# Optimization experiments

Measured on AMD Instinct MI355X. Metric: run time of the kernel, lower is better.

The kernel has to match this reference:

```python
import jax, jax.numpy as jnp
import numpy as np

N = 100_000   # entities
E = 1_000_000 # edges (triples)
R = 1_000     # relations
D = 100       # node_hidden
DEPTH = 2
EPS = 1e-12


def _segment_mean(vals, idx, num):
    s = jax.ops.segment_sum(vals, idx, num_segments=num)
    cnt = jax.ops.segment_sum(jnp.ones((vals.shape[0],), vals.dtype), idx, num_segments=num)
    return s / jnp.maximum(cnt, 1.0)[:, None]


def _edge_softmax(logits, dst, num):
    # softmax over edges grouped by destination node
    m = jax.ops.segment_max(logits, dst, num_segments=num)
    e = jnp.exp(logits - m[dst])
    s = jax.ops.segment_sum(e, dst, num_segments=num)
    return e / s[dst]


def _rrea_encoder(features, rel_emb, src, dst, erel, kernels):
    feats = jnp.tanh(features)
    outs = [feats]
    for l in range(DEPTH):
        rels = rel_emb[erel]                                        # [E, D]
        rels = rels / jnp.maximum(jnp.linalg.norm(rels, axis=1, keepdims=True), EPS)
        neighs = feats[src]                                         # [E, D]
        selfs = feats[dst]                                          # [E, D]
        # Householder reflection of neighbor features about relation direction
        neighs = neighs - 2.0 * jnp.sum(neighs * rels, axis=1, keepdims=True) * rels
        k = kernels[l]                                              # [3D, 1]
        w_s, w_n, w_r = k[:D, 0], k[D:2 * D, 0], k[2 * D:, 0]
        logits = selfs @ w_s + neighs @ w_n + rels @ w_r            # [E]
        att = _edge_softmax(logits, dst, N)
        feats = jax.ops.segment_sum(neighs * att[:, None], dst, num_segments=N)
        feats = jnp.tanh(feats)
        outs.append(feats)
    return jnp.concatenate(outs, axis=1)                            # [N, (DEPTH+1)*D]


def setup_inputs() -> dict:
    key = jax.random.key(0)
    k1, k2, k3, k4, k5, k6, k7 = jax.random.split(key, 7)
    ent_emb = jax.random.uniform(k1, (N, D), jnp.float32, -0.05, 0.05)
    rel_emb = jax.random.uniform(k2, (R, D), jnp.float32, -0.05, 0.05)
    attn_e = jax.random.normal(k3, (DEPTH, 3 * D, 1), jnp.float32)
    attn_r = jax.random.normal(k4, (DEPTH, 3 * D, 1), jnp.float32)
    src = jax.random.randint(k5, (E,), 0, N, jnp.int32)
    dst = jnp.sort(jax.random.randint(k6, (E,), 0, N, jnp.int32))
    erel = jax.random.randint(k7, (E,), 0, R, jnp.int32)
    return {"ent_emb": ent_emb, "rel_emb": rel_emb, "attn_e": attn_e,
            "attn_r": attn_r, "src": src, "dst": dst, "erel": erel}


def reference(ent_emb, rel_emb, attn_e, attn_r, src, dst, erel):
    # initial entity feature: mean of in-neighbor entity embeddings
    ent_feature = _segment_mean(ent_emb[src], dst, N)               # [N, D]
    # initial relation feature per entity: mean of incident relation embeddings
    rel_feature = _segment_mean(rel_emb[erel], dst, N)              # [N, D]
    out_ent = _rrea_encoder(ent_feature, rel_emb, src, dst, erel, attn_e)
    out_rel = _rrea_encoder(rel_feature, rel_emb, src, dst, erel, attn_r)
    # dropout_rate=0.0 / eval mode -> identity
    return jnp.concatenate([out_ent, out_rel], axis=-1)             # [N, 2*(DEPTH+1)*D]
```

## Files before the change

kernel.cpp:

```cpp
#include <hip/hip_runtime.h>
#include <hip/hip_fp16.h>
#include <math.h>

#define NN 100000
#define NE 1000000
#define NR 1000
#define DD 100
#define HS 104
#define FS2 208
#define OUTC 600
#define EPS 1e-12f
#define NBIN 64
#define RESCALE_THR 8.0f

struct __attribute__((aligned(16))) h8 { unsigned short u[8]; };

__device__ inline float h2f(unsigned short u) {
    __half_raw r; r.x = u; __half h = r; return __half2float(h);
}
__device__ inline unsigned short f2h(float f) {
    __half h = __float2half_rn(f); __half_raw r = h; return r.x;
}

__device__ inline float wave_sum(float v) {
#pragma unroll
    for (int o = 32; o > 0; o >>= 1) v += __shfl_down(v, o, 64);
    return __shfl(v, 0, 64);
}
__device__ inline float quad_sum(float v) {
    v += __shfl_xor(v, 1, 64);
    v += __shfl_xor(v, 2, 64);
    return v;
}

__global__ void k_rowptr(const int* __restrict__ dst, int* __restrict__ row_ptr,
                         int* __restrict__ ghist) {
    int n = blockIdx.x * blockDim.x + threadIdx.x;
    if (n < NBIN) ghist[n] = 0;
    if (n > NN) return;
    int lo = 0, hi = NE;
    while (lo < hi) {
        int mid = (lo + hi) >> 1;
        if (dst[mid] < n) lo = mid + 1; else hi = mid;
    }
    row_ptr[n] = lo;
}

__global__ void k_hist(const int* __restrict__ row_ptr, int* __restrict__ ghist) {
    __shared__ int lh[NBIN];
    int t = threadIdx.x;
    if (t < NBIN) lh[t] = 0;
    __syncthreads();
    int n = blockIdx.x * blockDim.x + t;
    if (n < NN) {
        int d = row_ptr[n + 1] - row_ptr[n];
        atomicAdd(&lh[min(d, NBIN - 1)], 1);
    }
    __syncthreads();
    if (t < NBIN && lh[t]) atomicAdd(&ghist[t], lh[t]);
}
__global__ void k_scan(const int* __restrict__ ghist, int* __restrict__ goffs) {
    if (threadIdx.x == 0) {
        int s = 0;
        for (int i = 0; i < NBIN; ++i) { goffs[i] = s; s += ghist[i]; }
    }
}
__global__ void k_scatter(const int* __restrict__ row_ptr, int* __restrict__ goffs,
                          int* __restrict__ perm) {
    __shared__ int lh[NBIN], base[NBIN];
    int t = threadIdx.x;
    if (t < NBIN) lh[t] = 0;
    __syncthreads();
    int n = blockIdx.x * blockDim.x + t;
    int bin = 0, rank = 0;
    if (n < NN) {
        int d = row_ptr[n + 1] - row_ptr[n];
        bin = min(d, NBIN - 1);
        rank = atomicAdd(&lh[bin], 1);
    }
    __syncthreads();
    if (t < NBIN && lh[t]) base[t] = atomicAdd(&goffs[t], lh[t]);
    __syncthreads();
    if (n < NN) perm[base[bin] + rank] = n;
}

__global__ void k_relnorm(const float* __restrict__ rel_emb, float* __restrict__ rel_norm,
                          unsigned short* __restrict__ rel_nh) {
    int w = (blockIdx.x * blockDim.x + threadIdx.x) >> 6;
    int lane = threadIdx.x & 63;
    if (w >= NR) return;
    const float* r = rel_emb + w * DD;
    float v0 = r[lane];
    float v1 = (lane + 64 < DD) ? r[lane + 64] : 0.f;
    float ss = wave_sum(v0 * v0 + v1 * v1);
    float sc = 1.f / fmaxf(sqrtf(ss), EPS);
    float* o = rel_norm + w * DD;
    unsigned short* oh = rel_nh + (size_t)w * HS;
    o[lane] = v0 * sc;
    oh[lane] = f2h(v0 * sc);
    if (lane + 64 < DD) {
        o[lane + 64] = v1 * sc;
        oh[lane + 64] = f2h(v1 * sc);
    }
}

__global__ void k_relv2(const float* __restrict__ rel_norm,
                        const float* __restrict__ k3dA, const float* __restrict__ k3dB,
                        float4* __restrict__ rrP) {
    int w = (blockIdx.x * blockDim.x + threadIdx.x) >> 6;
    int lane = threadIdx.x & 63;
    if (w >= NR) return;
    const float* r = rel_norm + w * DD;
    float r0 = r[lane];
    float r1 = (lane + 64 < DD) ? r[lane + 64] : 0.f;
    float wrA0 = k3dA[2 * DD + lane], wnA0 = k3dA[DD + lane];
    float wrB0 = k3dB[2 * DD + lane], wnB0 = k3dB[DD + lane];
    float wrA1 = 0.f, wnA1 = 0.f, wrB1 = 0.f, wnB1 = 0.f;
    if (lane + 64 < DD) {
        wrA1 = k3dA[2 * DD + lane + 64]; wnA1 = k3dA[DD + lane + 64];
        wrB1 = k3dB[2 * DD + lane + 64]; wnB1 = k3dB[DD + lane + 64];
    }
    float rdA = wave_sum(r0 * wrA0 + r1 * wrA1);
    float rdB = wave_sum(r0 * wrB0 + r1 * wrB1);
    float rnA = wave_sum(r0 * wnA0 + r1 * wnA1);
    float rnB = wave_sum(r0 * wnB0 + r1 * wnB1);
    if (lane == 0) { float4 v = { rdA, rdB, rnA, rnB }; rrP[w] = v; }
}


__global__ __launch_bounds__(256) void k_segmean2(
        const float* __restrict__ ent_emb, const float* __restrict__ rel_emb,
        const int* __restrict__ src, const int* __restrict__ erel,
        const int* __restrict__ row_ptr, const int* __restrict__ perm,
        const float* __restrict__ k3dA, const float* __restrict__ k3dB,
        float2* __restrict__ sdP, float2* __restrict__ ndP,
        unsigned short* __restrict__ fused_out,
        float* __restrict__ out) {
    int gi = (blockIdx.x * blockDim.x + threadIdx.x) >> 2;
    int sb = threadIdx.x & 3;
    if (gi >= NN) return;
    int n = perm[gi];
    int beg = row_ptr[n], end = row_ptr[n + 1];
    float a0[25] = {}, a1[25] = {};
    for (int e = beg; e < end; ++e) {
        int s = src[e];
        int t = erel[e];
        const float* er = ent_emb + (size_t)s * DD;
        const float* rr = rel_emb + (size_t)t * DD;
        const float4* e4 = (const float4*)er;
        const float4* r4 = (const float4*)rr;
#pragma unroll
        for (int k = 0; k < 6; ++k) {
            float4 v = e4[6 * sb + k];
            a0[4 * k] += v.x; a0[4 * k + 1] += v.y; a0[4 * k + 2] += v.z; a0[4 * k + 3] += v.w;
            float4 u = r4[6 * sb + k];
            a1[4 * k] += u.x; a1[4 * k + 1] += u.y; a1[4 * k + 2] += u.z; a1[4 * k + 3] += u.w;
        }
        a0[24] += er[96 + sb];
        a1[24] += rr[96 + sb];
    }
    float inv = 1.f / fmaxf((float)(end - beg), 1.f);
    float o0[25], o1[25];
#pragma unroll
    for (int m = 0; m < 25; ++m) { o0[m] = tanhf(a0[m] * inv); o1[m] = tanhf(a1[m] * inv); }
    if (fused_out) {
        unsigned short* fr = fused_out + (size_t)n * FS2;
#pragma unroll
        for (int j = 0; j < 3; ++j) {
            h8 x, y;
#pragma unroll
            for (int m = 0; m < 8; ++m) { x.u[m] = f2h(o0[8 * j + m]); y.u[m] = f2h(o1[8 * j + m]); }
            ((h8*)(fr + 24 * sb))[j] = x;
            ((h8*)(fr + 104 + 24 * sb))[j] = y;
        }
        fr[96 + sb] = f2h(o0[24]);
        fr[200 + sb] = f2h(o1[24]);
    }
    float* oc = out + (size_t)n * OUTC;
    float4* oc4 = (float4*)oc;
    float4* od4 = (float4*)(oc + 300);
#pragma unroll
    for (int k = 0; k < 6; ++k) {
        float4 v = { o0[4 * k], o0[4 * k + 1], o0[4 * k + 2], o0[4 * k + 3] };
        oc4[6 * sb + k] = v;
        float4 u = { o1[4 * k], o1[4 * k + 1], o1[4 * k + 2], o1[4 * k + 3] };
        od4[6 * sb + k] = u;
    }
    oc[96 + sb] = o0[24];
    oc[300 + 96 + sb] = o1[24];
    float sp0 = o0[24] * k3dA[96 + sb], np0 = o0[24] * k3dA[DD + 96 + sb];
    float sp1 = o1[24] * k3dB[96 + sb], np1 = o1[24] * k3dB[DD + 96 + sb];
    const float4* wA = (const float4*)k3dA;
    const float4* wAn = (const float4*)(k3dA + DD);
    const float4* wB = (const float4*)k3dB;
    const float4* wBn = (const float4*)(k3dB + DD);
#pragma unroll
    for (int k = 0; k < 6; ++k) {
        float4 ws = wA[6 * sb + k], wn = wAn[6 * sb + k];
        sp0 += o0[4 * k] * ws.x + o0[4 * k + 1] * ws.y + o0[4 * k + 2] * ws.z + o0[4 * k + 3] * ws.w;
        np0 += o0[4 * k] * wn.x + o0[4 * k + 1] * wn.y + o0[4 * k + 2] * wn.z + o0[4 * k + 3] * wn.w;
        float4 vs = wB[6 * sb + k], vn = wBn[6 * sb + k];
        sp1 += o1[4 * k] * vs.x + o1[4 * k + 1] * vs.y + o1[4 * k + 2] * vs.z + o1[4 * k + 3] * vs.w;
        np1 += o1[4 * k] * vn.x + o1[4 * k + 1] * vn.y + o1[4 * k + 2] * vn.z + o1[4 * k + 3] * vn.w;
    }
    sp0 = quad_sum(sp0); np0 = quad_sum(np0);
    sp1 = quad_sum(sp1); np1 = quad_sum(np1);
    if (sb == 0) {
        float2 sv = { sp0, sp1 }; sdP[n] = sv;
        float2 nv = { np0, np1 }; ndP[n] = nv;
    }
}

template<int SRC>
__global__ __launch_bounds__(256) void k_layer2(
        const void* __restrict__ Fin,
        const unsigned short* __restrict__ rel_nh,
        const int* __restrict__ src, const int* __restrict__ erel,
        const int* __restrict__ row_ptr, const int* __restrict__ perm,
        const float2* __restrict__ sdP, const float2* __restrict__ ndP,
        const float4* __restrict__ rrP,
        const float* __restrict__ k3dA_next, const float* __restrict__ k3dB_next,
        float2* __restrict__ sdP_o, float2* __restrict__ ndP_o,
        unsigned short* __restrict__ fused_out,
        float* __restrict__ out, int ocol) {
    int gi = (blockIdx.x * blockDim.x + threadIdx.x) >> 2;
    int sb = threadIdx.x & 3;
    if (gi >= NN) return;
    int n = perm[gi];
    int beg = row_ptr[n], end = row_ptr[n + 1];
    float2 sd2 = sdP[n];
    float acc0[25] = {}, acc1[25] = {};
    float m0 = -INFINITY, l0 = 0.f, m1 = -INFINITY, l1 = 0.f;
    for (int e = beg; e < end; ++e) {
        int s = src[e];
        int r = erel[e];
        float2 nd2 = ndP[s];
        float4 rr = rrP[r];
        float f0[25], f1[25], rv[25];
        if (SRC == 0) {
            const unsigned short* fr = (const unsigned short*)Fin + (size_t)s * FS2;
            const h8* p = (const h8*)(fr + 24 * sb);
            const h8* q = (const h8*)(fr + 104 + 24 * sb);
            h8 x0 = p[0], x1 = p[1], x2 = p[2];
            h8 y0 = q[0], y1 = q[1], y2 = q[2];
#pragma unroll
            for (int m = 0; m < 8; ++m) {
                f0[m] = h2f(x0.u[m]); f0[8 + m] = h2f(x1.u[m]); f0[16 + m] = h2f(x2.u[m]);
                f1[m] = h2f(y0.u[m]); f1[8 + m] = h2f(y1.u[m]); f1[16 + m] = h2f(y2.u[m]);
            }
            f0[24] = h2f(fr[96 + sb]);
            f1[24] = h2f(fr[200 + sb]);
        } else {
            const float* fr = (const float*)Fin + (size_t)s * OUTC;
            const float4* a4 = (const float4*)fr;
            const float4* b4 = (const float4*)(fr + 300);
#pragma unroll
            for (int k = 0; k < 6; ++k) {
                float4 v = a4[6 * sb + k];
                f0[4 * k] = v.x; f0[4 * k + 1] = v.y; f0[4 * k + 2] = v.z; f0[4 * k + 3] = v.w;
                float4 u = b4[6 * sb + k];
                f1[4 * k] = u.x; f1[4 * k + 1] = u.y; f1[4 * k + 2] = u.z; f1[4 * k + 3] = u.w;
            }
            f0[24] = fr[96 + sb];
            f1[24] = fr[300 + 96 + sb];
        }
        const unsigned short* rh = rel_nh + (size_t)r * HS;
        const h8* rp = (const h8*)(rh + 24 * sb);
        h8 z0 = rp[0], z1 = rp[1], z2 = rp[2];
#pragma unroll
        for (int m = 0; m < 8; ++m) {
            rv[m] = h2f(z0.u[m]); rv[8 + m] = h2f(z1.u[m]); rv[16 + m] = h2f(z2.u[m]);
        }
        rv[24] = h2f(rh[96 + sb]);
        float p0 = f0[24] * rv[24], p1 = f1[24] * rv[24];
#pragma unroll
        for (int m = 0; m < 24; ++m) { p0 += f0[m] * rv[m]; p1 += f1[m] * rv[m]; }
        p0 = quad_sum(p0);
        p1 = quad_sum(p1);
        float c0 = 2.f * p0, c1 = 2.f * p1;
        float lg0 = sd2.x + nd2.x - c0 * rr.z + rr.x;
        float lg1 = sd2.y + nd2.y - c1 * rr.w + rr.y;
        float w0, w1;
        if (lg0 > m0 + RESCALE_THR) {
            float sc = __expf(m0 - lg0);
            l0 *= sc;
#pragma unroll
            for (int m = 0; m < 25; ++m) acc0[m] *= sc;
            m0 = lg0; w0 = 1.f;
        } else w0 = __expf(lg0 - m0);
        if (lg1 > m1 + RESCALE_THR) {
            float sc = __expf(m1 - lg1);
            l1 *= sc;
#pragma unroll
            for (int m = 0; m < 25; ++m) acc1[m] *= sc;
            m1 = lg1; w1 = 1.f;
        } else w1 = __expf(lg1 - m1);
        l0 += w0; l1 += w1;
        float wc0 = w0 * c0, wc1 = w1 * c1;
#pragma unroll
        for (int m = 0; m < 25; ++m) {
            acc0[m] += w0 * f0[m] - wc0 * rv[m];
            acc1[m] += w1 * f1[m] - wc1 * rv[m];
        }
    }
    float i0 = (end > beg) ? (1.f / l0) : 0.f;
    float i1 = (end > beg) ? (1.f / l1) : 0.f;
    float o0[25], o1[25];
#pragma unroll
    for (int m = 0; m < 25; ++m) { o0[m] = tanhf(acc0[m] * i0); o1[m] = tanhf(acc1[m] * i1); }
    if (fused_out) {
        unsigned short* fr = fused_out + (size_t)n * FS2;
#pragma unroll
        for (int j = 0; j < 3; ++j) {
            h8 x, y;
#pragma unroll
            for (int m = 0; m < 8; ++m) { x.u[m] = f2h(o0[8 * j + m]); y.u[m] = f2h(o1[8 * j + m]); }
            ((h8*)(fr + 24 * sb))[j] = x;
            ((h8*)(fr + 104 + 24 * sb))[j] = y;
        }
        fr[96 + sb] = f2h(o0[24]);
        fr[200 + sb] = f2h(o1[24]);
    }
    float* oc = out + (size_t)n * OUTC + ocol;
    float4* oc4 = (float4*)oc;
    float4* od4 = (float4*)(oc + 300);
#pragma unroll
    for (int k = 0; k < 6; ++k) {
        float4 v = { o0[4 * k], o0[4 * k + 1], o0[4 * k + 2], o0[4 * k + 3] };
        oc4[6 * sb + k] = v;
        float4 u = { o1[4 * k], o1[4 * k + 1], o1[4 * k + 2], o1[4 * k + 3] };
        od4[6 * sb + k] = u;
    }
    oc[96 + sb] = o0[24];
    oc[300 + 96 + sb] = o1[24];
    if (k3dA_next) {
        float sp0 = o0[24] * k3dA_next[96 + sb], np0 = o0[24] * k3dA_next[DD + 96 + sb];
        float sp1 = o1[24] * k3dB_next[96 + sb], np1 = o1[24] * k3dB_next[DD + 96 + sb];
        const float4* wA = (const float4*)k3dA_next;
        const float4* wAn = (const float4*)(k3dA_next + DD);
        const float4* wB = (const float4*)k3dB_next;
        const float4* wBn = (const float4*)(k3dB_next + DD);
#pragma unroll
        for (int k = 0; k < 6; ++k) {
            float4 ws = wA[6 * sb + k], wn = wAn[6 * sb + k];
            sp0 += o0[4 * k] * ws.x + o0[4 * k + 1] * ws.y + o0[4 * k + 2] * ws.z + o0[4 * k + 3] * ws.w;
            np0 += o0[4 * k] * wn.x + o0[4 * k + 1] * wn.y + o0[4 * k + 2] * wn.z + o0[4 * k + 3] * wn.w;
            float4 vs = wB[6 * sb + k], vn = wBn[6 * sb + k];
            sp1 += o1[4 * k] * vs.x + o1[4 * k + 1] * vs.y + o1[4 * k + 2] * vs.z + o1[4 * k + 3] * vs.w;
            np1 += o1[4 * k] * vn.x + o1[4 * k + 1] * vn.y + o1[4 * k + 2] * vn.z + o1[4 * k + 3] * vn.w;
        }
        sp0 = quad_sum(sp0); np0 = quad_sum(np0);
        sp1 = quad_sum(sp1); np1 = quad_sum(np1);
        if (sb == 0) {
            float2 sv = { sp0, sp1 }; sdP_o[n] = sv;
            float2 nv = { np0, np1 }; ndP_o[n] = nv;
        }
    }
}

extern "C" void kernel_launch(void* const* d_in, const int* in_sizes, int n_in,
                              void* d_out, int out_size, void* d_ws, size_t ws_size,
                              hipStream_t stream) {
    const float* ent_emb = (const float*)d_in[0];
    const float* rel_emb = (const float*)d_in[1];
    const float* attn_e  = (const float*)d_in[2];
    const float* attn_r  = (const float*)d_in[3];
    const int*   src     = (const int*)d_in[4];
    const int*   dst     = (const int*)d_in[5];
    const int*   erel    = (const int*)d_in[6];
    float* out = (float*)d_out;

    char* ws = (char*)d_ws;
    size_t off = 0;
    auto alloc = [&](size_t bytes) -> void* {
        void* p = ws + off;
        off = (off + bytes + 255) & ~(size_t)255;
        return p;
    };
    int*    row_ptr  = (int*)alloc((NN + 1) * sizeof(int));
    float*  rel_norm = (float*)alloc((size_t)NR * DD * sizeof(float));
    unsigned short* rel_nh = (unsigned short*)alloc((size_t)NR * HS * sizeof(unsigned short));
    float2* sdPA = (float2*)alloc(NN * sizeof(float2));
    float2* ndPA = (float2*)alloc(NN * sizeof(float2));
    float2* sdPB = (float2*)alloc(NN * sizeof(float2));
    float2* ndPB = (float2*)alloc(NN * sizeof(float2));
    float4* rrP0 = (float4*)alloc(NR * sizeof(float4));
    float4* rrP1 = (float4*)alloc(NR * sizeof(float4));
    int*    ghist = (int*)alloc(NBIN * sizeof(int));
    int*    goffs = (int*)alloc(NBIN * sizeof(int));
    int*    perm  = (int*)alloc(NN * sizeof(int));
    unsigned short* fusedA = (unsigned short*)alloc((size_t)NN * FS2 * sizeof(unsigned short));
    bool planB = (off <= ws_size);
    unsigned short* fusedB = (unsigned short*)alloc((size_t)NN * FS2 * sizeof(unsigned short));
    bool planA = (off <= ws_size);

    hipLaunchKernelGGL(k_rowptr, dim3((NN + 256) / 256), dim3(256), 0, stream,
                       dst, row_ptr, ghist);
    hipLaunchKernelGGL(k_hist, dim3((NN + 255) / 256), dim3(256), 0, stream, row_ptr, ghist);
    hipLaunchKernelGGL(k_scan, dim3(1), dim3(64), 0, stream, ghist, goffs);
    hipLaunchKernelGGL(k_scatter, dim3((NN + 255) / 256), dim3(256), 0, stream,
                       row_ptr, goffs, perm);
    hipLaunchKernelGGL(k_relnorm, dim3(NR * 64 / 256), dim3(256), 0, stream,
                       rel_emb, rel_norm, rel_nh);
    hipLaunchKernelGGL(k_relv2, dim3(NR * 64 / 256), dim3(256), 0, stream,
                       rel_norm, attn_e, attn_r, rrP0);
    hipLaunchKernelGGL(k_relv2, dim3(NR * 64 / 256), dim3(256), 0, stream,
                       rel_norm, attn_e + 300, attn_r + 300, rrP1);

    const int NODE_BLOCKS = (NN + 63) / 64;

    hipLaunchKernelGGL(k_segmean2, dim3(NODE_BLOCKS), dim3(256), 0, stream,
                       ent_emb, rel_emb, src, erel, row_ptr, perm,
                       attn_e, attn_r, sdPA, ndPA,
                       planB ? fusedA : (unsigned short*)nullptr, out);

    if (planB) {
        hipLaunchKernelGGL(HIP_KERNEL_NAME(k_layer2<0>), dim3(NODE_BLOCKS), dim3(256), 0, stream,
                           (const void*)fusedA, rel_nh, src, erel, row_ptr, perm,
                           sdPA, ndPA, rrP0, attn_e + 300, attn_r + 300,
                           sdPB, ndPB,
                           planA ? fusedB : (unsigned short*)nullptr, out, 100);
    } else {
        hipLaunchKernelGGL(HIP_KERNEL_NAME(k_layer2<1>), dim3(NODE_BLOCKS), dim3(256), 0, stream,
                           (const void*)out, rel_nh, src, erel, row_ptr, perm,
                           sdPA, ndPA, rrP0, attn_e + 300, attn_r + 300,
                           sdPB, ndPB,
                           (unsigned short*)nullptr, out, 100);
    }

    if (planA) {
        hipLaunchKernelGGL(HIP_KERNEL_NAME(k_layer2<0>), dim3(NODE_BLOCKS), dim3(256), 0, stream,
                           (const void*)fusedB, rel_nh, src, erel, row_ptr, perm,
                           sdPB, ndPB, rrP1, (const float*)nullptr, (const float*)nullptr,
                           sdPB, ndPB,
                           (unsigned short*)nullptr, out, 200);
    } else {
        hipLaunchKernelGGL(HIP_KERNEL_NAME(k_layer2<1>), dim3(NODE_BLOCKS), dim3(256), 0, stream,
                           (const void*)(out + 100), rel_nh, src, erel, row_ptr, perm,
                           sdPB, ndPB, rrP1, (const float*)nullptr, (const float*)nullptr,
                           sdPB, ndPB,
                           (unsigned short*)nullptr, out, 200);
    }
}
```

Baseline: 760.6 us.

## Pack edge indices, gather fp16 embeddings, and schedule nodes via atomic work queue

```diff
diff --git a/kernel.cpp b/kernel.cpp
--- a/kernel.cpp
+++ b/kernel.cpp
@@ -12,6 +12,7 @@
 #define EPS 1e-12f
 #define NBIN 64
 #define RESCALE_THR 8.0f
+#define NWCH (NN / 16)
 
 struct __attribute__((aligned(16))) h8 { unsigned short u[8]; };
 
@@ -59,10 +60,12 @@
     __syncthreads();
     if (t < NBIN && lh[t]) atomicAdd(&ghist[t], lh[t]);
 }
-__global__ void k_scan(const int* __restrict__ ghist, int* __restrict__ goffs) {
+__global__ void k_scan(const int* __restrict__ ghist, int* __restrict__ goffs,
+                       int* __restrict__ ctrs) {
     if (threadIdx.x == 0) {
         int s = 0;
         for (int i = 0; i < NBIN; ++i) { goffs[i] = s; s += ghist[i]; }
+        ctrs[0] = 0; ctrs[1] = 0; ctrs[2] = 0;
     }
 }
 __global__ void k_scatter(const int* __restrict__ row_ptr, int* __restrict__ goffs,
@@ -82,6 +85,13 @@
     if (t < NBIN && lh[t]) base[t] = atomicAdd(&goffs[t], lh[t]);
     __syncthreads();
     if (n < NN) perm[base[bin] + rank] = n;
+}
+
+__global__ void k_pack(const int* __restrict__ src, const int* __restrict__ erel,
+                       unsigned int* __restrict__ ep) {
+    int e = blockIdx.x * blockDim.x + threadIdx.x;
+    if (e >= NE) return;
+    ep[e] = (unsigned int)src[e] | ((unsigned int)erel[e] << 17);
 }
 
 __global__ void k_relnorm(const float* __restrict__ rel_emb, float* __restrict__ rel_norm,
@@ -127,219 +137,101 @@
     if (lane == 0) { float4 v = { rdA, rdB, rnA, rnB }; rrP[w] = v; }
 }
 
+__global__ void k_tohalf(const float* __restrict__ s, unsigned short* __restrict__ d, int rows) {
+    int gi = blockIdx.x * blockDim.x + threadIdx.x;
+    int n = gi >> 2, sb = gi & 3;
+    if (n >= rows) return;
+    const float4* s4 = (const float4*)(s + (size_t)n * DD);
+    unsigned short* dr = d + (size_t)n * HS;
+#pragma unroll
+    for (int j = 0; j < 3; ++j) {
+        float4 a = s4[6 * sb + 2 * j];
+        float4 b = s4[6 * sb + 2 * j + 1];
+        h8 o;
+        o.u[0] = f2h(a.x); o.u[1] = f2h(a.y); o.u[2] = f2h(a.z); o.u[3] = f2h(a.w);
+        o.u[4] = f2h(b.x); o.u[5] = f2h(b.y); o.u[6] = f2h(b.z); o.u[7] = f2h(b.w);
+        ((h8*)(dr + 24 * sb))[j] = o;
+    }
+    dr[96 + sb] = f2h(s[(size_t)n * DD + 96 + sb]);
+}
+
 
 __global__ __launch_bounds__(256) void k_segmean2(
-        const float* __restrict__ ent_emb, const float* __restrict__ rel_emb,
-        const int* __restrict__ src, const int* __restrict__ erel,
+        const unsigned short* __restrict__ ent_h, const unsigned short* __restrict__ rel_eh,
+        const unsigned int* __restrict__ ep,
         const int* __restrict__ row_ptr, const int* __restrict__ perm,
         const float* __restrict__ k3dA, const float* __restrict__ k3dB,
         float2* __restrict__ sdP, float2* __restrict__ ndP,
         unsigned short* __restrict__ fused_out,
-        float* __restrict__ out) {
-    int gi = (blockIdx.x * blockDim.x + threadIdx.x) >> 2;
-    int sb = threadIdx.x & 3;
-    if (gi >= NN) return;
-    int n = perm[gi];
-    int beg = row_ptr[n], end = row_ptr[n + 1];
-    float a0[25] = {}, a1[25] = {};
-    for (int e = beg; e < end; ++e) {
-        int s = src[e];
-        int t = erel[e];
-        const float* er = ent_emb + (size_t)s * DD;
-        const float* rr = rel_emb + (size_t)t * DD;
-        const float4* e4 = (const float4*)er;
-        const float4* r4 = (const float4*)rr;
+        float* __restrict__ out, int* __restrict__ ctr) {
+    int lane = threadIdx.x & 63;
+    int qi = lane >> 2, sb = lane & 3;
+    for (;;) {
+        int t;
+        if (lane == 0) t = atomicAdd(ctr, 1);
+        t = __shfl(t, 0, 64);
+        if (t >= NWCH) break;
+        int gi = (NWCH - 1 - t) * 16 + qi;
+        int n = perm[gi];
+        int beg = row_ptr[n], end = row_ptr[n + 1];
+        float a0[25] = {}, a1[25] = {};
+        for (int e = beg; e < end; ++e) {
+            unsigned int v = ep[e];
+            int s = v & 0x1FFFF;
+            int r = v >> 17;
+            const unsigned short* er = ent_h + (size_t)s * HS;
+            const unsigned short* rr = rel_eh + (size_t)r * HS;
+            const h8* e8 = (const h8*)(er + 24 * sb);
+            const h8* r8 = (const h8*)(rr + 24 * sb);
+            h8 xa = e8[0], xb = e8[1], xc = e8[2];
+            h8 ya = r8[0], yb = r8[1], yc = r8[2];
+#pragma unroll
+            for (int m = 0; m < 8; ++m) {
+                a0[m]      += h2f(xa.u[m]);
+                a0[8 + m]  += h2f(xb.u[m]);
+                a0[16 + m] += h2f(xc.u[m]);
+                a1[m]      += h2f(ya.u[m]);
+                a1[8 + m]  += h2f(yb.u[m]);
+                a1[16 + m] += h2f(yc.u[m]);
+            }
+            a0[24] += h2f(er[96 + sb]);
+            a1[24] += h2f(rr[96 + sb]);
+        }
+        float inv = 1.f / fmaxf((float)(end - beg), 1.f);
+        float o0[25], o1[25];
+#pragma unroll
+        for (int m = 0; m < 25; ++m) { o0[m] = tanhf(a0[m] * inv); o1[m] = tanhf(a1[m] * inv); }
+        if (fused_out) {
+            unsigned short* fr = fused_out + (size_t)n * FS2;
+#pragma unroll
+            for (int j = 0; j < 3; ++j) {
+                h8 x, y;
+#pragma unroll
+                for (int m = 0; m < 8; ++m) { x.u[m] = f2h(o0[8 * j + m]); y.u[m] = f2h(o1[8 * j + m]); }
+                ((h8*)(fr + 24 * sb))[j] = x;
+                ((h8*)(fr + 104 + 24 * sb))[j] = y;
+            }
+            fr[96 + sb] = f2h(o0[24]);
+            fr[200 + sb] = f2h(o1[24]);
+        }
+        float* oc = out + (size_t)n * OUTC;
+        float4* oc4 = (float4*)oc;
+        float4* od4 = (float4*)(oc + 300);
 #pragma unroll
         for (int k = 0; k < 6; ++k) {
-            float4 v = e4[6 * sb + k];
-            a0[4 * k] += v.x; a0[4 * k + 1] += v.y; a0[4 * k + 2] += v.z; a0[4 * k + 3] += v.w;
-            float4 u = r4[6 * sb + k];
-            a1[4 * k] += u.x; a1[4 * k + 1] += u.y; a1[4 * k + 2] += u.z; a1[4 * k + 3] += u.w;
-        }
-        a0[24] += er[96 + sb];
-        a1[24] += rr[96 + sb];
-    }
-    float inv = 1.f / fmaxf((float)(end - beg), 1.f);
-    float o0[25], o1[25];
-#pragma unroll
-    for (int m = 0; m < 25; ++m) { o0[m] = tanhf(a0[m] * inv); o1[m] = tanhf(a1[m] * inv); }
-    if (fused_out) {
-        unsigned short* fr = fused_out + (size_t)n * FS2;
-#pragma unroll
-        for (int j = 0; j < 3; ++j) {
-            h8 x, y;
-#pragma unroll
-            for (int m = 0; m < 8; ++m) { x.u[m] = f2h(o0[8 * j + m]); y.u[m] = f2h(o1[8 * j + m]); }
-            ((h8*)(fr + 24 * sb))[j] = x;
-            ((h8*)(fr + 104 + 24 * sb))[j] = y;
-        }
-        fr[96 + sb] = f2h(o0[24]);
-        fr[200 + sb] = f2h(o1[24]);
-    }
-    float* oc = out + (size_t)n * OUTC;
-    float4* oc4 = (float4*)oc;
-    float4* od4 = (float4*)(oc + 300);
-#pragma unroll
-    for (int k = 0; k < 6; ++k) {
-        float4 v = { o0[4 * k], o0[4 * k + 1], o0[4 * k + 2], o0[4 * k + 3] };
-        oc4[6 * sb + k] = v;
-        float4 u = { o1[4 * k], o1[4 * k + 1], o1[4 * k + 2], o1[4 * k + 3] };
-        od4[6 * sb + k] = u;
-    }
-    oc[96 + sb] = o0[24];
-    oc[300 + 96 + sb] = o1[24];
-    float sp0 = o0[24] * k3dA[96 + sb], np0 = o0[24] * k3dA[DD + 96 + sb];
-    float sp1 = o1[24] * k3dB[96 + sb], np1 = o1[24] * k3dB[DD + 96 + sb];
-    const float4* wA = (const float4*)k3dA;
-    const float4* wAn = (const float4*)(k3dA + DD);
-    const float4* wB = (const float4*)k3dB;
-    const float4* wBn = (const float4*)(k3dB + DD);
-#pragma unroll
-    for (int k = 0; k < 6; ++k) {
-        float4 ws = wA[6 * sb + k], wn = wAn[6 * sb + k];
-        sp0 += o0[4 * k] * ws.x + o0[4 * k + 1] * ws.y + o0[4 * k + 2] * ws.z + o0[4 * k + 3] * ws.w;
-        np0 += o0[4 * k] * wn.x + o0[4 * k + 1] * wn.y + o0[4 * k + 2] * wn.z + o0[4 * k + 3] * wn.w;
-        float4 vs = wB[6 * sb + k], vn = wBn[6 * sb + k];
-        sp1 += o1[4 * k] * vs.x + o1[4 * k + 1] * vs.y + o1[4 * k + 2] * vs.z + o1[4 * k + 3] * vs.w;
-        np1 += o1[4 * k] * vn.x + o1[4 * k + 1] * vn.y + o1[4 * k + 2] * vn.z + o1[4 * k + 3] * vn.w;
-    }
-    sp0 = quad_sum(sp0); np0 = quad_sum(np0);
-    sp1 = quad_sum(sp1); np1 = quad_sum(np1);
-    if (sb == 0) {
-        float2 sv = { sp0, sp1 }; sdP[n] = sv;
-        float2 nv = { np0, np1 }; ndP[n] = nv;
-    }
-}
-
-template<int SRC>
-__global__ __launch_bounds__(256) void k_layer2(
-        const void* __restrict__ Fin,
-        const unsigned short* __restrict__ rel_nh,
-        const int* __restrict__ src, const int* __restrict__ erel,
-        const int* __restrict__ row_ptr, const int* __restrict__ perm,
-        const float2* __restrict__ sdP, const float2* __restrict__ ndP,
-        const float4* __restrict__ rrP,
-        const float* __restrict__ k3dA_next, const float* __restrict__ k3dB_next,
-        float2* __restrict__ sdP_o, float2* __restrict__ ndP_o,
-        unsigned short* __restrict__ fused_out,
-        float* __restrict__ out, int ocol) {
-    int gi = (blockIdx.x * blockDim.x + threadIdx.x) >> 2;
-    int sb = threadIdx.x & 3;
-    if (gi >= NN) return;
-    int n = perm[gi];
-    int beg = row_ptr[n], end = row_ptr[n + 1];
-    float2 sd2 = sdP[n];
-    float acc0[25] = {}, acc1[25] = {};
-    float m0 = -INFINITY, l0 = 0.f, m1 = -INFINITY, l1 = 0.f;
-    for (int e = beg; e < end; ++e) {
-        int s = src[e];
-        int r = erel[e];
-        float2 nd2 = ndP[s];
-        float4 rr = rrP[r];
-        float f0[25], f1[25], rv[25];
-        if (SRC == 0) {
-            const unsigned short* fr = (const unsigned short*)Fin + (size_t)s * FS2;
-            const h8* p = (const h8*)(fr + 24 * sb);
-            const h8* q = (const h8*)(fr + 104 + 24 * sb);
-            h8 x0 = p[0], x1 = p[1], x2 = p[2];
-            h8 y0 = q[0], y1 = q[1], y2 = q[2];
-#pragma unroll
-            for (int m = 0; m < 8; ++m) {
-                f0[m] = h2f(x0.u[m]); f0[8 + m] = h2f(x1.u[m]); f0[16 + m] = h2f(x2.u[m]);
-                f1[m] = h2f(y0.u[m]); f1[8 + m] = h2f(y1.u[m]); f1[16 + m] = h2f(y2.u[m]);
-            }
-            f0[24] = h2f(fr[96 + sb]);
-            f1[24] = h2f(fr[200 + sb]);
-        } else {
-            const float* fr = (const float*)Fin + (size_t)s * OUTC;
-            const float4* a4 = (const float4*)fr;
-            const float4* b4 = (const float4*)(fr + 300);
-#pragma unroll
-            for (int k = 0; k < 6; ++k) {
-                float4 v = a4[6 * sb + k];
-                f0[4 * k] = v.x; f0[4 * k + 1] = v.y; f0[4 * k + 2] = v.z; f0[4 * k + 3] = v.w;
-                float4 u = b4[6 * sb + k];
-                f1[4 * k] = u.x; f1[4 * k + 1] = u.y; f1[4 * k + 2] = u.z; f1[4 * k + 3] = u.w;
-            }
-            f0[24] = fr[96 + sb];
-            f1[24] = fr[300 + 96 + sb];
-        }
-        const unsigned short* rh = rel_nh + (size_t)r * HS;
-        const h8* rp = (const h8*)(rh + 24 * sb);
-        h8 z0 = rp[0], z1 = rp[1], z2 = rp[2];
-#pragma unroll
-        for (int m = 0; m < 8; ++m) {
-            rv[m] = h2f(z0.u[m]); rv[8 + m] = h2f(z1.u[m]); rv[16 + m] = h2f(z2.u[m]);
-        }
-        rv[24] = h2f(rh[96 + sb]);
-        float p0 = f0[24] * rv[24], p1 = f1[24] * rv[24];
-#pragma unroll
-        for (int m = 0; m < 24; ++m) { p0 += f0[m] * rv[m]; p1 += f1[m] * rv[m]; }
-        p0 = quad_sum(p0);
-        p1 = quad_sum(p1);
-        float c0 = 2.f * p0, c1 = 2.f * p1;
-        float lg0 = sd2.x + nd2.x - c0 * rr.z + rr.x;
-        float lg1 = sd2.y + nd2.y - c1 * rr.w + rr.y;
-        float w0, w1;
-        if (lg0 > m0 + RESCALE_THR) {
-            float sc = __expf(m0 - lg0);
-            l0 *= sc;
-#pragma unroll
-            for (int m = 0; m < 25; ++m) acc0[m] *= sc;
-            m0 = lg0; w0 = 1.f;
-        } else w0 = __expf(lg0 - m0);
-        if (lg1 > m1 + RESCALE_THR) {
-            float sc = __expf(m1 - lg1);
-            l1 *= sc;
-#pragma unroll
-            for (int m = 0; m < 25; ++m) acc1[m] *= sc;
-            m1 = lg1; w1 = 1.f;
-        } else w1 = __expf(lg1 - m1);
-        l0 += w0; l1 += w1;
-        float wc0 = w0 * c0, wc1 = w1 * c1;
-#pragma unroll
-        for (int m = 0; m < 25; ++m) {
-            acc0[m] += w0 * f0[m] - wc0 * rv[m];
-            acc1[m] += w1 * f1[m] - wc1 * rv[m];
-        }
-    }
-    float i0 = (end > beg) ? (1.f / l0) : 0.f;
-    float i1 = (end > beg) ? (1.f / l1) : 0.f;
-    float o0[25], o1[25];
-#pragma unroll
-    for (int m = 0; m < 25; ++m) { o0[m] = tanhf(acc0[m] * i0); o1[m] = tanhf(acc1[m] * i1); }
-    if (fused_out) {
-        unsigned short* fr = fused_out + (size_t)n * FS2;
-#pragma unroll
-        for (int j = 0; j < 3; ++j) {
-            h8 x, y;
-#pragma unroll
-            for (int m = 0; m < 8; ++m) { x.u[m] = f2h(o0[8 * j + m]); y.u[m] = f2h(o1[8 * j + m]); }
-            ((h8*)(fr + 24 * sb))[j] = x;
-            ((h8*)(fr + 104 + 24 * sb))[j] = y;
-        }
-        fr[96 + sb] = f2h(o0[24]);
-        fr[200 + sb] = f2h(o1[24]);
-    }
-    float* oc = out + (size_t)n * OUTC + ocol;
-    float4* oc4 = (float4*)oc;
-    float4* od4 = (float4*)(oc + 300);
-#pragma unroll
-    for (int k = 0; k < 6; ++k) {
-        float4 v = { o0[4 * k], o0[4 * k + 1], o0[4 * k + 2], o0[4 * k + 3] };
-        oc4[6 * sb + k] = v;
-        float4 u = { o1[4 * k], o1[4 * k + 1], o1[4 * k + 2], o1[4 * k + 3] };
-        od4[6 * sb + k] = u;
-    }
-    oc[96 + sb] = o0[24];
-    oc[300 + 96 + sb] = o1[24];
-    if (k3dA_next) {
-        float sp0 = o0[24] * k3dA_next[96 + sb], np0 = o0[24] * k3dA_next[DD + 96 + sb];
-        float sp1 = o1[24] * k3dB_next[96 + sb], np1 = o1[24] * k3dB_next[DD + 96 + sb];
-        const float4* wA = (const float4*)k3dA_next;
-        const float4* wAn = (const float4*)(k3dA_next + DD);
-        const float4* wB = (const float4*)k3dB_next;
-        const float4* wBn = (const float4*)(k3dB_next + DD);
+            float4 v0 = { o0[4 * k], o0[4 * k + 1], o0[4 * k + 2], o0[4 * k + 3] };
+            oc4[6 * sb + k] = v0;
+            float4 u0 = { o1[4 * k], o1[4 * k + 1], o1[4 * k + 2], o1[4 * k + 3] };
+            od4[6 * sb + k] = u0;
+        }
+        oc[96 + sb] = o0[24];
+        oc[300 + 96 + sb] = o1[24];
+        float sp0 = o0[24] * k3dA[96 + sb], np0 = o0[24] * k3dA[DD + 96 + sb];
+        float sp1 = o1[24] * k3dB[96 + sb], np1 = o1[24] * k3dB[DD + 96 + sb];
+        const float4* wA = (const float4*)k3dA;
+        const float4* wAn = (const float4*)(k3dA + DD);
+        const float4* wB = (const float4*)k3dB;
+        const float4* wBn = (const float4*)(k3dB + DD);
 #pragma unroll
         for (int k = 0; k < 6; ++k) {
             float4 ws = wA[6 * sb + k], wn = wAn[6 * sb + k];
@@ -352,8 +244,162 @@
         sp0 = quad_sum(sp0); np0 = quad_sum(np0);
         sp1 = quad_sum(sp1); np1 = quad_sum(np1);
         if (sb == 0) {
-            float2 sv = { sp0, sp1 }; sdP_o[n] = sv;
-            float2 nv = { np0, np1 }; ndP_o[n] = nv;
+            float2 sv = { sp0, sp1 }; sdP[n] = sv;
+            float2 nv = { np0, np1 }; ndP[n] = nv;
+        }
+    }
+}
+
+template<int SRC>
+__global__ __launch_bounds__(256) void k_layer2(
+        const void* __restrict__ Fin,
+        const unsigned short* __restrict__ rel_nh,
+        const unsigned int* __restrict__ ep,
+        const int* __restrict__ row_ptr, const int* __restrict__ perm,
+        const float2* __restrict__ sdP, const float2* __restrict__ ndP,
+        const float4* __restrict__ rrP,
+        const float* __restrict__ k3dA_next, const float* __restrict__ k3dB_next,
+        float2* __restrict__ sdP_o, float2* __restrict__ ndP_o,
+        unsigned short* __restrict__ fused_out,
+        float* __restrict__ out, int ocol, int* __restrict__ ctr) {
+    int lane = threadIdx.x & 63;
+    int qi = lane >> 2, sb = lane & 3;
+    for (;;) {
+        int tk;
+        if (lane == 0) tk = atomicAdd(ctr, 1);
+        tk = __shfl(tk, 0, 64);
+        if (tk >= NWCH) break;
+        int gi = (NWCH - 1 - tk) * 16 + qi;
+        int n = perm[gi];
+        int beg = row_ptr[n], end = row_ptr[n + 1];
+        float2 sd2 = sdP[n];
+        float acc0[25] = {}, acc1[25] = {};
+        float m0 = -INFINITY, l0 = 0.f, m1 = -INFINITY, l1 = 0.f;
+        for (int e = beg; e < end; ++e) {
+            unsigned int v = ep[e];
+            int s = v & 0x1FFFF;
+            int r = v >> 17;
+            float2 nd2 = ndP[s];
+            float4 rr = rrP[r];
+            float f0[25], f1[25], rv[25];
+            if (SRC == 0) {
+                const unsigned short* fr = (const unsigned short*)Fin + (size_t)s * FS2;
+                const h8* p = (const h8*)(fr + 24 * sb);
+                const h8* q = (const h8*)(fr + 104 + 24 * sb);
+                h8 x0 = p[0], x1 = p[1], x2 = p[2];
+                h8 y0 = q[0], y1 = q[1], y2 = q[2];
+#pragma unroll
+                for (int m = 0; m < 8; ++m) {
+                    f0[m] = h2f(x0.u[m]); f0[8 + m] = h2f(x1.u[m]); f0[16 + m] = h2f(x2.u[m]);
+                    f1[m] = h2f(y0.u[m]); f1[8 + m] = h2f(y1.u[m]); f1[16 + m] = h2f(y2.u[m]);
+                }
+                f0[24] = h2f(fr[96 + sb]);
+                f1[24] = h2f(fr[200 + sb]);
+            } else {
+                const float* fr = (const float*)Fin + (size_t)s * OUTC;
+                const float4* a4 = (const float4*)fr;
+                const float4* b4 = (const float4*)(fr + 300);
+#pragma unroll
+                for (int k = 0; k < 6; ++k) {
+                    float4 vv = a4[6 * sb + k];
+                    f0[4 * k] = vv.x; f0[4 * k + 1] = vv.y; f0[4 * k + 2] = vv.z; f0[4 * k + 3] = vv.w;
+                    float4 uu = b4[6 * sb + k];
+                    f1[4 * k] = uu.x; f1[4 * k + 1] = uu.y; f1[4 * k + 2] = uu.z; f1[4 * k + 3] = uu.w;
+                }
+                f0[24] = fr[96 + sb];
+                f1[24] = fr[300 + 96 + sb];
+            }
+            const unsigned short* rh = rel_nh + (size_t)r * HS;
+            const h8* rp = (const h8*)(rh + 24 * sb);
+            h8 z0 = rp[0], z1 = rp[1], z2 = rp[2];
+#pragma unroll
+            for (int m = 0; m < 8; ++m) {
+                rv[m] = h2f(z0.u[m]); rv[8 + m] = h2f(z1.u[m]); rv[16 + m] = h2f(z2.u[m]);
+            }
+            rv[24] = h2f(rh[96 + sb]);
+            float p0 = f0[24] * rv[24], p1 = f1[24] * rv[24];
+#pragma unroll
+            for (int m = 0; m < 24; ++m) { p0 += f0[m] * rv[m]; p1 += f1[m] * rv[m]; }
+            p0 = quad_sum(p0);
+            p1 = quad_sum(p1);
+            float c0 = 2.f * p0, c1 = 2.f * p1;
+            float lg0 = sd2.x + nd2.x - c0 * rr.z + rr.x;
+            float lg1 = sd2.y + nd2.y - c1 * rr.w + rr.y;
+            float w0, w1;
+            if (lg0 > m0 + RESCALE_THR) {
+                float sc = __expf(m0 - lg0);
+                l0 *= sc;
+#pragma unroll
+                for (int m = 0; m < 25; ++m) acc0[m] *= sc;
+                m0 = lg0; w0 = 1.f;
+            } else w0 = __expf(lg0 - m0);
+            if (lg1 > m1 + RESCALE_THR) {
+                float sc = __expf(m1 - lg1);
+                l1 *= sc;
+#pragma unroll
+                for (int m = 0; m < 25; ++m) acc1[m] *= sc;
+                m1 = lg1; w1 = 1.f;
+            } else w1 = __expf(lg1 - m1);
+            l0 += w0; l1 += w1;
+            float wc0 = w0 * c0, wc1 = w1 * c1;
+#pragma unroll
+            for (int m = 0; m < 25; ++m) {
+                acc0[m] += w0 * f0[m] - wc0 * rv[m];
+                acc1[m] += w1 * f1[m] - wc1 * rv[m];
+            }
+        }
+        float i0 = (end > beg) ? (1.f / l0) : 0.f;
+        float i1 = (end > beg) ? (1.f / l1) : 0.f;
+        float o0[25], o1[25];
+#pragma unroll
+        for (int m = 0; m < 25; ++m) { o0[m] = tanhf(acc0[m] * i0); o1[m] = tanhf(acc1[m] * i1); }
+        if (fused_out) {
+            unsigned short* fr = fused_out + (size_t)n * FS2;
+#pragma unroll
+            for (int j = 0; j < 3; ++j) {
+                h8 x, y;
+#pragma unroll
+                for (int m = 0; m < 8; ++m) { x.u[m] = f2h(o0[8 * j + m]); y.u[m] = f2h(o1[8 * j + m]); }
+                ((h8*)(fr + 24 * sb))[j] = x;
+                ((h8*)(fr + 104 + 24 * sb))[j] = y;
+            }
+            fr[96 + sb] = f2h(o0[24]);
+            fr[200 + sb] = f2h(o1[24]);
+        }
+        float* oc = out + (size_t)n * OUTC + ocol;
+        float4* oc4 = (float4*)oc;
+        float4* od4 = (float4*)(oc + 300);
+#pragma unroll
+        for (int k = 0; k < 6; ++k) {
+            float4 vv = { o0[4 * k], o0[4 * k + 1], o0[4 * k + 2], o0[4 * k + 3] };
+            oc4[6 * sb + k] = vv;
+            float4 uu = { o1[4 * k], o1[4 * k + 1], o1[4 * k + 2], o1[4 * k + 3] };
+            od4[6 * sb + k] = uu;
+        }
+        oc[96 + sb] = o0[24];
+        oc[300 + 96 + sb] = o1[24];
+        if (k3dA_next) {
+            float sp0 = o0[24] * k3dA_next[96 + sb], np0 = o0[24] * k3dA_next[DD + 96 + sb];
+            float sp1 = o1[24] * k3dB_next[96 + sb], np1 = o1[24] * k3dB_next[DD + 96 + sb];
+            const float4* wA = (const float4*)k3dA_next;
+            const float4* wAn = (const float4*)(k3dA_next + DD);
+            const float4* wB = (const float4*)k3dB_next;
+            const float4* wBn = (const float4*)(k3dB_next + DD);
+#pragma unroll
+            for (int k = 0; k < 6; ++k) {
+                float4 ws = wA[6 * sb + k], wn = wAn[6 * sb + k];
+                sp0 += o0[4 * k] * ws.x + o0[4 * k + 1] * ws.y + o0[4 * k + 2] * ws.z + o0[4 * k + 3] * ws.w;
+                np0 += o0[4 * k] * wn.x + o0[4 * k + 1] * wn.y + o0[4 * k + 2] * wn.z + o0[4 * k + 3] * wn.w;
+                float4 vs = wB[6 * sb + k], vn = wBn[6 * sb + k];
+                sp1 += o1[4 * k] * vs.x + o1[4 * k + 1] * vs.y + o1[4 * k + 2] * vs.z + o1[4 * k + 3] * vs.w;
+                np1 += o1[4 * k] * vn.x + o1[4 * k + 1] * vn.y + o1[4 * k + 2] * vn.z + o1[4 * k + 3] * vn.w;
+            }
+            sp0 = quad_sum(sp0); np0 = quad_sum(np0);
+            sp1 = quad_sum(sp1); np1 = quad_sum(np1);
+            if (sb == 0) {
+                float2 sv = { sp0, sp1 }; sdP_o[n] = sv;
+                float2 nv = { np0, np1 }; ndP_o[n] = nv;
+            }
         }
     }
 }
@@ -371,74 +417,84 @@
     float* out = (float*)d_out;
 
     char* ws = (char*)d_ws;
-    size_t off = 0;
-    auto alloc = [&](size_t bytes) -> void* {
-        void* p = ws + off;
-        off = (off + bytes + 255) & ~(size_t)255;
-        return p;
-    };
-    int*    row_ptr  = (int*)alloc((NN + 1) * sizeof(int));
-    float*  rel_norm = (float*)alloc((size_t)NR * DD * sizeof(float));
-    unsigned short* rel_nh = (unsigned short*)alloc((size_t)NR * HS * sizeof(unsigned short));
-    float2* sdPA = (float2*)alloc(NN * sizeof(float2));
-    float2* ndPA = (float2*)alloc(NN * sizeof(float2));
-    float2* sdPB = (float2*)alloc(NN * sizeof(float2));
-    float2* ndPB = (float2*)alloc(NN * sizeof(float2));
-    float4* rrP0 = (float4*)alloc(NR * sizeof(float4));
-    float4* rrP1 = (float4*)alloc(NR * sizeof(float4));
-    int*    ghist = (int*)alloc(NBIN * sizeof(int));
-    int*    goffs = (int*)alloc(NBIN * sizeof(int));
-    int*    perm  = (int*)alloc(NN * sizeof(int));
-    unsigned short* fusedA = (unsigned short*)alloc((size_t)NN * FS2 * sizeof(unsigned short));
-    bool planB = (off <= ws_size);
-    unsigned short* fusedB = (unsigned short*)alloc((size_t)NN * FS2 * sizeof(unsigned short));
-    bool planA = (off <= ws_size);
+    auto al = [](size_t x) { return (x + 255) & ~(size_t)255; };
+    size_t o = 0;
+    auto take = [&](size_t bytes) -> void* { void* p = ws + o; o = al(o + bytes); return p; };
+
+    int*    row_ptr = (int*)take((NN + 1) * sizeof(int));
+    unsigned short* rel_nh = (unsigned short*)take((size_t)NR * HS * 2);
+    float2* sdPA = (float2*)take(NN * sizeof(float2));
+    float2* ndPA = (float2*)take(NN * sizeof(float2));
+    float2* sdPB = (float2*)take(NN * sizeof(float2));
+    float2* ndPB = (float2*)take(NN * sizeof(float2));
+    float4* rrP0 = (float4*)take(NR * sizeof(float4));
+    float4* rrP1 = (float4*)take(NR * sizeof(float4));
+    int*    ghist = (int*)take(NBIN * sizeof(int));
+    int*    goffs = (int*)take(NBIN * sizeof(int));
+    int*    perm  = (int*)take(NN * sizeof(int));
+    int*    ctrs  = (int*)take(3 * sizeof(int));
+    unsigned int* ep = (unsigned int*)take((size_t)NE * 4);
+
+    size_t tbl0 = o;
+    size_t tbl1 = al(tbl0 + (size_t)NN * HS * 2);
+    size_t tbl2 = al(tbl1 + (size_t)NR * HS * 2);
+    size_t tblE = al(tbl2 + (size_t)NR * DD * 4);
+    size_t fsz  = al((size_t)NN * FS2 * 2);
+    size_t tblSpan = tblE - tbl0;
+    size_t fA_A = tbl0 + (fsz > tblSpan ? fsz : tblSpan);
+    bool planA = (fA_A + fsz) <= ws_size;
+    size_t fA_off = planA ? fA_A : tblE;
+    bool haveFA = planA || ((tblE + fsz) <= ws_size);
+
+    unsigned short* ent_h  = (unsigned short*)(ws + tbl0);
+    unsigned short* rel_eh = (unsigned short*)(ws + tbl1);
+    float*          rel_norm = (float*)(ws + tbl2);
+    unsigned short* fusedA = haveFA ? (unsigned short*)(ws + fA_off) : (unsigned short*)nullptr;
+    unsigned short* fusedB = planA ? (unsigned short*)(ws + tbl0) : (unsigned short*)nullptr;
 
     hipLaunchKernelGGL(k_rowptr, dim3((NN + 256) / 256), dim3(256), 0, stream,
                        dst, row_ptr, ghist);
     hipLaunchKernelGGL(k_hist, dim3((NN + 255) / 256), dim3(256), 0, stream, row_ptr, ghist);
-    hipLaunchKernelGGL(k_scan, dim3(1), dim3(64), 0, stream, ghist, goffs);
+    hipLaunchKernelGGL(k_scan, dim3(1), dim3(64), 0, stream, ghist, goffs, ctrs);
     hipLaunchKernelGGL(k_scatter, dim3((NN + 255) / 256), dim3(256), 0, stream,
                        row_ptr, goffs, perm);
+    hipLaunchKernelGGL(k_pack, dim3((NE + 255) / 256), dim3(256), 0, stream, src, erel, ep);
     hipLaunchKernelGGL(k_relnorm, dim3(NR * 64 / 256), dim3(256), 0, stream,
                        rel_emb, rel_norm, rel_nh);
     hipLaunchKernelGGL(k_relv2, dim3(NR * 64 / 256), dim3(256), 0, stream,
                        rel_norm, attn_e, attn_r, rrP0);
     hipLaunchKernelGGL(k_relv2, dim3(NR * 64 / 256), dim3(256), 0, stream,
                        rel_norm, attn_e + 300, attn_r + 300, rrP1);
-
-    const int NODE_BLOCKS = (NN + 63) / 64;
-
-    hipLaunchKernelGGL(k_segmean2, dim3(NODE_BLOCKS), dim3(256), 0, stream,
-                       ent_emb, rel_emb, src, erel, row_ptr, perm,
-                       attn_e, attn_r, sdPA, ndPA,
-                       planB ? fusedA : (unsigned short*)nullptr, out);
-
-    if (planB) {
-        hipLaunchKernelGGL(HIP_KERNEL_NAME(k_layer2<0>), dim3(NODE_BLOCKS), dim3(256), 0, stream,
-                           (const void*)fusedA, rel_nh, src, erel, row_ptr, perm,
+    hipLaunchKernelGGL(k_tohalf, dim3((NN * 4 + 255) / 256), dim3(256), 0, stream,
+                       ent_emb, ent_h, NN);
+    hipLaunchKernelGGL(k_tohalf, dim3((NR * 4 + 255) / 256), dim3(256), 0, stream,
+                       rel_emb, rel_eh, NR);
+
+    hipLaunchKernelGGL(k_segmean2, dim3(2048), dim3(256), 0, stream,
+                       ent_h, rel_eh, ep, row_ptr, perm,
+                       attn_e, attn_r, sdPA, ndPA, fusedA, out, ctrs + 0);
+
+    if (haveFA) {
+        hipLaunchKernelGGL(HIP_KERNEL_NAME(k_layer2<0>), dim3(1024), dim3(256), 0, stream,
+                           (const void*)fusedA, rel_nh, ep, row_ptr, perm,
                            sdPA, ndPA, rrP0, attn_e + 300, attn_r + 300,
-                           sdPB, ndPB,
-                           planA ? fusedB : (unsigned short*)nullptr, out, 100);
+                           sdPB, ndPB, fusedB, out, 100, ctrs + 1);
     } else {
-        hipLaunchKernelGGL(HIP_KERNEL_NAME(k_layer2<1>), dim3(NODE_BLOCKS), dim3(256), 0, stream,
-                           (const void*)out, rel_nh, src, erel, row_ptr, perm,
+        hipLaunchKernelGGL(HIP_KERNEL_NAME(k_layer2<1>), dim3(1024), dim3(256), 0, stream,
+                           (const void*)out, rel_nh, ep, row_ptr, perm,
                            sdPA, ndPA, rrP0, attn_e + 300, attn_r + 300,
-                           sdPB, ndPB,
-                           (unsigned short*)nullptr, out, 100);
+                           sdPB, ndPB, (unsigned short*)nullptr, out, 100, ctrs + 1);
     }
 
     if (planA) {
-        hipLaunchKernelGGL(HIP_KERNEL_NAME(k_layer2<0>), dim3(NODE_BLOCKS), dim3(256), 0, stream,
-                           (const void*)fusedB, rel_nh, src, erel, row_ptr, perm,
+        hipLaunchKernelGGL(HIP_KERNEL_NAME(k_layer2<0>), dim3(1024), dim3(256), 0, stream,
+                           (const void*)fusedB, rel_nh, ep, row_ptr, perm,
                            sdPB, ndPB, rrP1, (const float*)nullptr, (const float*)nullptr,
-                           sdPB, ndPB,
-                           (unsigned short*)nullptr, out, 200);
+                           sdPB, ndPB, (unsigned short*)nullptr, out, 200, ctrs + 2);
     } else {
-        hipLaunchKernelGGL(HIP_KERNEL_NAME(k_layer2<1>), dim3(NODE_BLOCKS), dim3(256), 0, stream,
-                           (const void*)(out + 100), rel_nh, src, erel, row_ptr, perm,
+        hipLaunchKernelGGL(HIP_KERNEL_NAME(k_layer2<1>), dim3(1024), dim3(256), 0, stream,
+                           (const void*)(out + 100), rel_nh, ep, row_ptr, perm,
                            sdPB, ndPB, rrP1, (const float*)nullptr, (const float*)nullptr,
-                           sdPB, ndPB,
-                           (unsigned short*)nullptr, out, 200);
-    }
-}
+                           sdPB, ndPB, (unsigned short*)nullptr, out, 200, ctrs + 2);
+    }
+}
```

Measured after the change: 883.0 us. +16.1%, slower.
